# Performance work log

Measured on AMD Instinct MI355X. Metric: run time of the kernel, lower is better.

The kernel has to match this reference:

```python
import jax, jax.numpy as jnp
import numpy as np
import math

D_DIM = 512
N_HEAD = 8
HIDDEN = 2048
N_LAYERS = 4
CONTEXT = 64
MAX_LEN = 5000


def make_pe(d_model, max_len=MAX_LEN):
    position = np.arange(max_len)[:, None].astype(np.float32)
    div_term = np.exp(np.arange(0, d_model, 2).astype(np.float32) * (-math.log(10000.0) / d_model))
    pe = np.zeros((max_len, d_model), dtype=np.float32)
    pe[:, 0::2] = np.sin(position * div_term)
    pe[:, 1::2] = np.cos(position * div_term)
    return jnp.asarray(pe)


def setup_inputs() -> dict:
    key = jax.random.key(0)
    ks = jax.random.split(key, 64)
    B, T, IN = 16, 2048, 512
    inp = {}
    inp["trajectory"] = jax.random.normal(ks[0], (B, T, IN), dtype=jnp.float32)
    inp["obs_length"] = jax.random.randint(ks[1], (B,), 0, T)
    s = 0.02
    inp["w_in"] = jax.random.normal(ks[2], (IN, D_DIM), dtype=jnp.float32) * s
    inp["b_in"] = jnp.zeros((D_DIM,), dtype=jnp.float32)
    # per-layer params
    params = []
    ki = 3
    for l in range(N_LAYERS):
        p = {}
        p["w_qkv"] = jax.random.normal(ks[ki], (D_DIM, 3 * D_DIM), dtype=jnp.float32) * s; ki += 1
        p["b_qkv"] = jnp.zeros((3 * D_DIM,), dtype=jnp.float32)
        p["w_o"] = jax.random.normal(ks[ki], (D_DIM, D_DIM), dtype=jnp.float32) * s; ki += 1
        p["b_o"] = jnp.zeros((D_DIM,), dtype=jnp.float32)
        p["w_ff1"] = jax.random.normal(ks[ki], (D_DIM, HIDDEN), dtype=jnp.float32) * s; ki += 1
        p["b_ff1"] = jnp.zeros((HIDDEN,), dtype=jnp.float32)
        p["w_ff2"] = jax.random.normal(ks[ki], (HIDDEN, D_DIM), dtype=jnp.float32) * s; ki += 1
        p["b_ff2"] = jnp.zeros((D_DIM,), dtype=jnp.float32)
        p["ln1_g"] = jnp.ones((D_DIM,), dtype=jnp.float32)
        p["ln1_b"] = jnp.zeros((D_DIM,), dtype=jnp.float32)
        p["ln2_g"] = jnp.ones((D_DIM,), dtype=jnp.float32)
        p["ln2_b"] = jnp.zeros((D_DIM,), dtype=jnp.float32)
        for name, v in p.items():
            inp[f"L{l}_{name}"] = v
    return inp


def layer_norm(x, g, b, eps=1e-5):
    mu = jnp.mean(x, axis=-1, keepdims=True)
    var = jnp.mean((x - mu) ** 2, axis=-1, keepdims=True)
    return (x - mu) * jax.lax.rsqrt(var + eps) * g + b


def build_attn_mask(T, obs_length, context_length):
    # boolean mask, True = masked out. Causal + per-sample context window.
    i = jnp.arange(T)[:, None]
    j = jnp.arange(T)[None, :]
    causal = j > i  # (T, T)
    # window restriction applies for rows i with context_length < i < obs_length:
    # mask positions j <= i - context_length - 1, i.e. j < i - context_length
    window = j < (i - context_length)  # (T,T)
    row_active = (i[None, :, :] > context_length) & (i[None, :, :] < obs_length[:, None, None])  # (B,T,1)
    mask = causal[None] | (window[None] & row_active)  # (B,T,T)
    return mask


def encoder_layer(x, mask_add, pad_bool, p):
    B, T, D = x.shape
    H = N_HEAD
    Dh = D // H
    qkv = x @ p["w_qkv"] + p["b_qkv"]  # (B,T,3D)
    q, k, v = jnp.split(qkv, 3, axis=-1)
    q = q.reshape(B, T, H, Dh).transpose(0, 2, 1, 3)
    k = k.reshape(B, T, H, Dh).transpose(0, 2, 1, 3)
    v = v.reshape(B, T, H, Dh).transpose(0, 2, 1, 3)
    scores = jnp.einsum("bhqd,bhkd->bhqk", q, k) / jnp.sqrt(jnp.float32(Dh))
    scores = scores + mask_add[:, None] + pad_bool[:, None, None, :] * jnp.float32(-1e9)
    attn = jax.nn.softmax(scores, axis=-1)
    ctx = jnp.einsum("bhqk,bhkd->bhqd", attn, v)
    ctx = ctx.transpose(0, 2, 1, 3).reshape(B, T, D)
    attn_out = ctx @ p["w_o"] + p["b_o"]
    x = layer_norm(x + attn_out, p["ln1_g"], p["ln1_b"])
    ff = jax.nn.relu(x @ p["w_ff1"] + p["b_ff1"]) @ p["w_ff2"] + p["b_ff2"]
    x = layer_norm(x + ff, p["ln2_g"], p["ln2_b"])
    return x


def reference(trajectory, obs_length, w_in, b_in,
              L0_w_qkv, L0_b_qkv, L0_w_o, L0_b_o, L0_w_ff1, L0_b_ff1, L0_w_ff2, L0_b_ff2, L0_ln1_g, L0_ln1_b, L0_ln2_g, L0_ln2_b,
              L1_w_qkv, L1_b_qkv, L1_w_o, L1_b_o, L1_w_ff1, L1_b_ff1, L1_w_ff2, L1_b_ff2, L1_ln1_g, L1_ln1_b, L1_ln2_g, L1_ln2_b,
              L2_w_qkv, L2_b_qkv, L2_w_o, L2_b_o, L2_w_ff1, L2_b_ff1, L2_w_ff2, L2_b_ff2, L2_ln1_g, L2_ln1_b, L2_ln2_g, L2_ln2_b,
              L3_w_qkv, L3_b_qkv, L3_w_o, L3_b_o, L3_w_ff1, L3_b_ff1, L3_w_ff2, L3_b_ff2, L3_ln1_g, L3_ln1_b, L3_ln2_g, L3_ln2_b):
    B, T, _ = trajectory.shape
    pad = jnp.arange(T)[None, :] > obs_length[:, None]  # (B,T) True = pad
    x = trajectory @ w_in + b_in
    x = x + make_pe(D_DIM)[None, :T]
    mask_bool = build_attn_mask(T, obs_length, CONTEXT)  # (B,T,T)
    mask_add = jnp.where(mask_bool, jnp.float32(-1e9), jnp.float32(0.0))
    layers = [
        dict(w_qkv=L0_w_qkv, b_qkv=L0_b_qkv, w_o=L0_w_o, b_o=L0_b_o, w_ff1=L0_w_ff1, b_ff1=L0_b_ff1, w_ff2=L0_w_ff2, b_ff2=L0_b_ff2, ln1_g=L0_ln1_g, ln1_b=L0_ln1_b, ln2_g=L0_ln2_g, ln2_b=L0_ln2_b),
        dict(w_qkv=L1_w_qkv, b_qkv=L1_b_qkv, w_o=L1_w_o, b_o=L1_b_o, w_ff1=L1_w_ff1, b_ff1=L1_b_ff1, w_ff2=L1_w_ff2, b_ff2=L1_b_ff2, ln1_g=L1_ln1_g, ln1_b=L1_ln1_b, ln2_g=L1_ln2_g, ln2_b=L1_ln2_b),
        dict(w_qkv=L2_w_qkv, b_qkv=L2_b_qkv, w_o=L2_w_o, b_o=L2_b_o, w_ff1=L2_w_ff1, b_ff1=L2_b_ff1, w_ff2=L2_w_ff2, b_ff2=L2_b_ff2, ln1_g=L2_ln1_g, ln1_b=L2_ln1_b, ln2_g=L2_ln2_g, ln2_b=L2_ln2_b),
        dict(w_qkv=L3_w_qkv, b_qkv=L3_b_qkv, w_o=L3_w_o, b_o=L3_b_o, w_ff1=L3_w_ff1, b_ff1=L3_b_ff1, w_ff2=L3_w_ff2, b_ff2=L3_b_ff2, ln1_g=L3_ln1_g, ln1_b=L3_ln1_b, ln2_g=L3_ln2_g, ln2_b=L3_ln2_b),
    ]
    for p in layers:
        x = encoder_layer(x, mask_add, pad, p)
    # aggregate
    keep = ~pad
    x = x * keep[:, :, None]
    denom = jnp.sum(keep, axis=1).astype(x.dtype)[:, None]
    return jnp.sum(x, axis=1) / denom
```

## Files before the change

kernel.cpp:

```cpp
#include <hip/hip_runtime.h>

typedef unsigned short u16;
typedef unsigned int u32;
typedef __bf16 bf16x8 __attribute__((ext_vector_type(8)));
typedef float f32x4 __attribute__((ext_vector_type(4)));

#define MFMA16(a, b, c) __builtin_amdgcn_mfma_f32_16x16x32_bf16((a), (b), (c), 0, 0, 0)

__device__ __forceinline__ u16 f2bf(float x) {
    union { float f; u32 u; } v; v.f = x;
    u32 r = v.u + 0x7fffu + ((v.u >> 16) & 1u);
    return (u16)(r >> 16);
}
__device__ __forceinline__ float bf2f(u16 x) {
    union { u32 u; float f; } v; v.u = ((u32)x) << 16; return v.f;
}

typedef const __attribute__((address_space(1))) u32* gas1_t;
typedef __attribute__((address_space(3))) u32* las3_t;
__device__ __forceinline__ void g2lds16(const void* g, void* l) {
    __builtin_amdgcn_global_load_lds((gas1_t)g, (las3_t)l, 16, 0, 0);
}

template <int MODE, int BK>
__global__ __launch_bounds__(256) void gemm_bf16(
    const u16* __restrict__ A, const u16* __restrict__ BT,
    const float* __restrict__ bias, float* __restrict__ outF,
    u16* __restrict__ outB, const float* __restrict__ aux,
    const int* __restrict__ obs,
    int M, int N, int K)
{
    __shared__ u16 As[2][128 * BK];
    __shared__ u16 Bs[2][128 * BK];
    const int tid = threadIdx.x;
    const int w = tid >> 6, l = tid & 63;
    const int gx = gridDim.x, gy = gridDim.y;
    const int orig = blockIdx.y * gx + blockIdx.x;
    int tm, tn;
    if ((gy & 15) == 0) {
        const int xcd = orig & 7;
        const int loc = orig >> 3;
        tn = loc % gx;
        const int j = loc / gx;
        const int bb = j >> 1;
        tm = bb * 16 + ((xcd - bb) & 7) + ((j & 1) << 3);
    } else {
        tm = blockIdx.y; tn = blockIdx.x;
    }
    const int bm = tm * 128, bn = tn * 128;
    if ((bm & 2047) > obs[bm >> 11]) return;
    const int wr = (w >> 1) * 64, wc = (w & 1) * 64;
    f32x4 acc[4][4] = {};
    const int lane15 = l & 15, lhi = l >> 4;

    const int larow = l >> 2, lacol = (l & 3) * 8;
    const int r0a = 16 * w, r0b = 16 * (w + 4);
    const u16* Ap = &A[(size_t)(bm + larow) * K + lacol];
    const u16* Bp = &BT[(size_t)(bn + larow) * K + lacol];
    const int srow = l >> 3;
    const int scol = ((l & 7) ^ srow) << 3;

    auto STAGE = [&](int buf, int kt) {
        if constexpr (BK == 32) {
            g2lds16(Ap + (size_t)r0a * K + kt, &As[buf][r0a * 32]);
            g2lds16(Bp + (size_t)r0a * K + kt, &Bs[buf][r0a * 32]);
            g2lds16(Ap + (size_t)r0b * K + kt, &As[buf][r0b * 32]);
            g2lds16(Bp + (size_t)r0b * K + kt, &Bs[buf][r0b * 32]);
        } else {
            #pragma unroll
            for (int q = 0; q < 4; ++q) {
                const int rr = w * 32 + q * 8;
                g2lds16(&A[(size_t)(bm + rr + srow) * K + kt + scol], &As[buf][rr * 64]);
                g2lds16(&BT[(size_t)(bn + rr + srow) * K + kt + scol], &Bs[buf][rr * 64]);
            }
        }
    };

    STAGE(0, 0);
    __syncthreads();
    int cur = 0;
    const int nk = K / BK;
    for (int ki = 0; ki < nk; ++ki) {
        if (ki + 1 < nk) STAGE(cur ^ 1, (ki + 1) * BK);
        if constexpr (BK == 32) {
            bf16x8 af[4], bfr[4];
            #pragma unroll
            for (int i = 0; i < 4; ++i)
                af[i] = *(const bf16x8*)&As[cur][(wr + i * 16 + lane15) * 32 + 8 * lhi];
            #pragma unroll
            for (int j = 0; j < 4; ++j)
                bfr[j] = *(const bf16x8*)&Bs[cur][(wc + j * 16 + lane15) * 32 + 8 * lhi];
            #pragma unroll
            for (int i = 0; i < 4; ++i)
                #pragma unroll
                for (int j = 0; j < 4; ++j)
                    acc[i][j] = MFMA16(af[i], bfr[j], acc[i][j]);
        } else {
            #pragma unroll
            for (int kk = 0; kk < 2; ++kk) {
                const int gsw = ((kk * 4 + lhi) ^ (l & 7)) << 3;
                bf16x8 af[4], bfr[4];
                #pragma unroll
                for (int i = 0; i < 4; ++i)
                    af[i] = *(const bf16x8*)&As[cur][(wr + i * 16 + lane15) * 64 + gsw];
                #pragma unroll
                for (int j = 0; j < 4; ++j)
                    bfr[j] = *(const bf16x8*)&Bs[cur][(wc + j * 16 + lane15) * 64 + gsw];
                #pragma unroll
                for (int i = 0; i < 4; ++i)
                    #pragma unroll
                    for (int j = 0; j < 4; ++j)
                        acc[i][j] = MFMA16(af[i], bfr[j], acc[i][j]);
            }
        }
        __syncthreads();
        cur ^= 1;
    }

    const int r0 = bm + wr + lhi * 4;
    const int c0 = bn + wc + lane15;
    #pragma unroll
    for (int i = 0; i < 4; ++i) {
        #pragma unroll
        for (int j = 0; j < 4; ++j) {
            const int col = c0 + j * 16;
            const float bc = bias[col];
            #pragma unroll
            for (int r = 0; r < 4; ++r) {
                const int row = r0 + i * 16 + r;
                const size_t idx = (size_t)row * N + col;
                float val = acc[i][j][r] + bc;
                if constexpr (MODE == 0) {
                    val += aux[(size_t)(row & 2047) * 512 + col];
                    outF[idx] = val;
                    outB[idx] = f2bf(val);
                } else if constexpr (MODE == 1) {
                    outB[idx] = f2bf(val);
                } else if constexpr (MODE == 2) {
                    outF[idx] = val + aux[idx];
                } else {
                    outB[idx] = f2bf(fmaxf(val, 0.f));
                }
            }
        }
    }
}

__global__ void pe_kernel(float* __restrict__ PE) {
    const int idx = blockIdx.x * 256 + threadIdx.x;
    const int t = idx >> 8, p = idx & 255;
    const float fr = expf((float)(2 * p) * -0.017988946039015984f);
    const float arg = (float)t * fr;
    float s, c;
    sincosf(arg, &s, &c);
    float2 v = {s, c};
    *(float2*)&PE[(size_t)t * 512 + 2 * p] = v;
}

__global__ __launch_bounds__(256) void attn_kernel(
    const u16* __restrict__ QKV, u16* __restrict__ CTX, const int* __restrict__ obs,
    float* __restrict__ PBm, float* __restrict__ PBl, float* __restrict__ PBo)
{
    __shared__ u16 Ks[64 * 64];
    __shared__ u16 Vt[64 * 64];
    __shared__ u16 Ps[4][16 * 64];
    const int b = blockIdx.z, h = blockIdx.y;
    const int L = obs[b];
    const int tid = threadIdx.x, w = tid >> 6, l = tid & 63;
    const size_t tb = (size_t)b * 2048;

    if (blockIdx.x >= 32) {
        const int cbase = (blockIdx.x - 32) * 4;
        if (cbase * 64 > L) return;
        const int cc = cbase + w;
        float* pP = (float*)Ks;
        u16 q16[64];
        #pragma unroll
        for (int dd = 0; dd < 8; ++dd)
            *(uint4*)&q16[dd * 8] = *(const uint4*)&QKV[(tb + L) * 1536 + h * 64 + dd * 8];
        const int j = cc * 64 + l;
        const bool val = (j <= L);
        float s = -3.0e38f;
        if (val) {
            s = 0.f;
            const u16* kp = &QKV[(tb + j) * 1536 + 512 + h * 64];
            #pragma unroll
            for (int dd = 0; dd < 8; ++dd) {
                uint4 kk = *(const uint4*)&kp[dd * 8];
                const u16* ke = (const u16*)&kk;
                #pragma unroll
                for (int e = 0; e < 8; ++e)
                    s += bf2f(q16[dd * 8 + e]) * bf2f(ke[e]);
            }
            s *= 0.125f;
        }
        float mx = s;
        #pragma unroll
        for (int d = 1; d < 64; d <<= 1) mx = fmaxf(mx, __shfl_xor(mx, d, 64));
        const float p = val ? __expf(s - mx) : 0.f;
        float ps = p;
        #pragma unroll
        for (int d = 1; d < 64; d <<= 1) ps += __shfl_xor(ps, d, 64);
        pP[w * 64 + l] = p;
        __builtin_amdgcn_wave_barrier();
        if (cc * 64 <= L) {
            float oacc = 0.f;
            #pragma unroll 4
            for (int jj = 0; jj < 64; ++jj) {
                const int key = cc * 64 + jj;
                const int rr = (key <= L) ? key : L;
                oacc += pP[w * 64 + jj] * bf2f(QKV[(tb + rr) * 1536 + 1024 + h * 64 + l]);
            }
            const int pidx = (b * 8 + h) * 32 + cc;
            PBo[(size_t)pidx * 64 + l] = oacc;
            if (l == 0) { PBm[pidx] = mx; PBl[pidx] = ps; }
        }
        return;
    }

    const int i0 = blockIdx.x * 64;
    if (i0 > L) return;

    bf16x8 qa0, qa1;
    {
        const int qrow = i0 + 16 * w + (l & 15);
        const u16* qp = &QKV[(tb + qrow) * 1536 + h * 64];
        qa0 = *(const bf16x8*)(qp + 8 * (l >> 4));
        qa1 = *(const bf16x8*)(qp + 32 + 8 * (l >> 4));
    }
    const int g0 = (l >> 4) ^ (l & 7);
    const int g1 = ((l >> 4) + 4) ^ (l & 7);

    float m_r[4] = {-1e30f, -1e30f, -1e30f, -1e30f};
    float l_r[4] = {0.f, 0.f, 0.f, 0.f};
    f32x4 acc_o[4] = {};
    const int klo = (i0 >= 128) ? (i0 - 64) : 0;
    int khi = (L < klo) ? klo : min(i0 + 63, L);

    for (int j0 = klo; j0 <= khi; j0 += 64) {
        __syncthreads();
        {
            const int krow0 = 8 * w + (l >> 3);
            const int kswz = ((l & 7) ^ (l >> 3)) << 3;
            #pragma unroll
            for (int q = 0; q < 2; ++q) {
                const int row = krow0 + 32 * q;
                g2lds16(&QKV[(tb + j0 + row) * 1536 + 512 + h * 64 + kswz],
                        &Ks[(8 * w + 32 * q) * 64]);
            }
            const int vr = tid >> 3, c8 = (tid & 7) * 8;
            #pragma unroll
            for (int q = 0; q < 2; ++q) {
                const int row = vr + 32 * q;
                uint4 vv = *(const uint4*)&QKV[(tb + j0 + row) * 1536 + 1024 + h * 64 + c8];
                const u16* vs = (const u16*)&vv;
                #pragma unroll
                for (int e = 0; e < 8; ++e) {
                    const int d = c8 + e;
                    Vt[d * 64 + (((row >> 3) ^ e) << 3) + (row & 7)] = vs[e];
                }
            }
        }
        __syncthreads();
        f32x4 s[4];
        #pragma unroll
        for (int f = 0; f < 4; ++f) {
            f32x4 z = {0.f, 0.f, 0.f, 0.f};
            const int rowk = (f * 16 + (l & 15)) * 64;
            bf16x8 kb0 = *(const bf16x8*)&Ks[rowk + g0 * 8];
            bf16x8 kb1 = *(const bf16x8*)&Ks[rowk + g1 * 8];
            z = MFMA16(qa0, kb0, z);
            z = MFMA16(qa1, kb1, z);
            s[f] = z;
        }
        float pm[4];
        #pragma unroll
        for (int r = 0; r < 4; ++r) {
            const int i_r = i0 + 16 * w + (l >> 4) * 4 + r;
            float mx = -__builtin_inff();
            #pragma unroll
            for (int f = 0; f < 4; ++f) {
                const int j = j0 + f * 16 + (l & 15);
                float sv = s[f][r] * 0.125f;
                const bool ok = (i_r >= L) ? (j == klo)
                              : (j <= i_r && (i_r <= 64 || j >= i_r - 64));
                sv = ok ? sv : -__builtin_inff();
                s[f][r] = sv;
                mx = fmaxf(mx, sv);
            }
            pm[r] = mx;
        }
        #pragma unroll
        for (int d = 1; d < 16; d <<= 1)
            #pragma unroll
            for (int r = 0; r < 4; ++r) pm[r] = fmaxf(pm[r], __shfl_xor(pm[r], d, 64));
        float sc[4];
        #pragma unroll
        for (int r = 0; r < 4; ++r) {
            const float mn = fmaxf(m_r[r], fmaxf(pm[r], -1e30f));
            sc[r] = __expf(m_r[r] - mn);
            m_r[r] = mn;
            l_r[r] *= sc[r];
        }
        #pragma unroll
        for (int f = 0; f < 4; ++f)
            #pragma unroll
            for (int r = 0; r < 4; ++r) acc_o[f][r] *= sc[r];
        float ps[4] = {0.f, 0.f, 0.f, 0.f};
        #pragma unroll
        for (int f = 0; f < 4; ++f)
            #pragma unroll
            for (int r = 0; r < 4; ++r) {
                const float p = __expf(s[f][r] - m_r[r]);
                s[f][r] = p;
                ps[r] += p;
            }
        #pragma unroll
        for (int d = 1; d < 16; d <<= 1)
            #pragma unroll
            for (int r = 0; r < 4; ++r) ps[r] += __shfl_xor(ps[r], d, 64);
        #pragma unroll
        for (int r = 0; r < 4; ++r) l_r[r] += ps[r];
        {
            const int cg = ((l >> 3) & 1);
            #pragma unroll
            for (int f = 0; f < 4; ++f)
                #pragma unroll
                for (int r = 0; r < 4; ++r) {
                    const int prow = (l >> 4) * 4 + r;
                    Ps[w][prow * 64 + (((f * 2 + cg) ^ (prow & 7)) << 3) + (l & 7)] =
                        f2bf(s[f][r]);
                }
        }
        bf16x8 pa0 = *(const bf16x8*)&Ps[w][(l & 15) * 64 + g0 * 8];
        bf16x8 pa1 = *(const bf16x8*)&Ps[w][(l & 15) * 64 + g1 * 8];
        #pragma unroll
        for (int f = 0; f < 4; ++f) {
            const int dv = (f * 16 + (l & 15)) * 64;
            bf16x8 vb0 = *(const bf16x8*)&Vt[dv + g0 * 8];
            bf16x8 vb1 = *(const bf16x8*)&Vt[dv + g1 * 8];
            acc_o[f] = MFMA16(pa0, vb0, acc_o[f]);
            acc_o[f] = MFMA16(pa1, vb1, acc_o[f]);
        }
    }
    #pragma unroll
    for (int r = 0; r < 4; ++r) {
        const float inv = 1.f / l_r[r];
        const int row = i0 + 16 * w + (l >> 4) * 4 + r;
        if (row != L) {
            #pragma unroll
            for (int f = 0; f < 4; ++f)
                CTX[(tb + row) * 512 + h * 64 + f * 16 + (l & 15)] = f2bf(acc_o[f][r] * inv);
        }
    }
}

__global__ void attn_merge(const float* __restrict__ PBm, const float* __restrict__ PBl,
                           const float* __restrict__ PBo, u16* __restrict__ CTX,
                           const int* __restrict__ obs)
{
    const int h = blockIdx.x, b = blockIdx.y, l = threadIdx.x;
    const int L = obs[b];
    const int nc = (L >> 6) + 1;
    const int base = (b * 8 + h) * 32;
    float m = -3.0e38f;
    for (int c = 0; c < nc; ++c) m = fmaxf(m, PBm[base + c]);
    float lt = 0.f, ot = 0.f;
    for (int c = 0; c < nc; ++c) {
        const float sc = __expf(PBm[base + c] - m);
        lt += sc * PBl[base + c];
        ot += sc * PBo[(size_t)(base + c) * 64 + l];
    }
    CTX[((size_t)b * 2048 + L) * 512 + h * 64 + l] = f2bf(ot / lt);
}

__global__ __launch_bounds__(256) void ln_kernel(
    const float* __restrict__ Y, const float* __restrict__ gw,
    const float* __restrict__ bw, float* __restrict__ X, u16* __restrict__ Xb,
    const int* __restrict__ obs)
{
    const int tok0 = blockIdx.x * 4;
    if ((tok0 & 2047) > obs[tok0 >> 11]) return;
    const int tok = tok0 + (threadIdx.x >> 6);
    const int l = threadIdx.x & 63;
    const float* y = &Y[(size_t)tok * 512 + l * 8];
    f32x4 v0 = *(const f32x4*)y;
    f32x4 v1 = *(const f32x4*)(y + 4);
    float s = 0.f, sq = 0.f;
    #pragma unroll
    for (int e = 0; e < 4; ++e) {
        s += v0[e] + v1[e];
        sq += v0[e] * v0[e] + v1[e] * v1[e];
    }
    #pragma unroll
    for (int d = 1; d < 64; d <<= 1) {
        s += __shfl_xor(s, d, 64);
        sq += __shfl_xor(sq, d, 64);
    }
    const float mean = s * (1.f / 512.f);
    const float var = sq * (1.f / 512.f) - mean * mean;
    const float rstd = rsqrtf(var + 1e-5f);
    f32x4 o0, o1;
    union { u16 us[8]; uint4 u4; } pk;
    #pragma unroll
    for (int e = 0; e < 8; ++e) {
        const int d = l * 8 + e;
        const float xv = (e < 4) ? v0[e] : v1[e - 4];
        const float ov = (xv - mean) * rstd * gw[d] + bw[d];
        if (e < 4) o0[e] = ov; else o1[e - 4] = ov;
        pk.us[e] = f2bf(ov);
    }
    float* xo = &X[(size_t)tok * 512 + l * 8];
    *(f32x4*)xo = o0;
    *(f32x4*)(xo + 4) = o1;
    *(uint4*)&Xb[(size_t)tok * 512 + l * 8] = pk.u4;
}

__global__ void cast_bf16_kernel(const float* __restrict__ in, u16* __restrict__ out, int n) {
    const int i = (blockIdx.x * 256 + threadIdx.x) * 4;
    if (i + 3 < n) {
        f32x4 v = *(const f32x4*)&in[i];
        union { u16 us[4]; uint2 u2; } pk;
        #pragma unroll
        for (int e = 0; e < 4; ++e) pk.us[e] = f2bf(v[e]);
        *(uint2*)&out[i] = pk.u2;
    }
}

__global__ void transpose_cast(const float* __restrict__ W, u16* __restrict__ WT, int K, int N) {
    __shared__ float t[32][33];
    const int n0 = blockIdx.x * 32, k0 = blockIdx.y * 32;
    const int tx = threadIdx.x, ty = threadIdx.y;
    #pragma unroll
    for (int r = 0; r < 32; r += 8)
        t[ty + r][tx] = W[(size_t)(k0 + ty + r) * N + n0 + tx];
    __syncthreads();
    #pragma unroll
    for (int r = 0; r < 32; r += 8)
        WT[(size_t)(n0 + ty + r) * K + k0 + tx] = f2bf(t[tx][ty + r]);
}

struct WPack { const float* src[16]; u16* dst[16]; };
__global__ void transpose_all(WPack p) {
    __shared__ float t[32][33];
    int id = blockIdx.x;
    const int lyr = id / 3072;
    id -= lyr * 3072;
    int wi, K, N;
    if (id < 768)       { wi = 0; K = 512;  N = 1536; }
    else if (id < 1024) { wi = 1; K = 512;  N = 512;  id -= 768; }
    else if (id < 2048) { wi = 2; K = 512;  N = 2048; id -= 1024; }
    else                { wi = 3; K = 2048; N = 512;  id -= 2048; }
    const float* W = p.src[lyr * 4 + wi];
    u16* D = p.dst[lyr * 4 + wi];
    const int nx = N >> 5;
    const int n0 = (id % nx) * 32, k0 = (id / nx) * 32;
    const int tx = threadIdx.x, ty = threadIdx.y;
    #pragma unroll
    for (int r = 0; r < 32; r += 8)
        t[ty + r][tx] = W[(size_t)(k0 + ty + r) * N + n0 + tx];
    __syncthreads();
    #pragma unroll
    for (int r = 0; r < 32; r += 8)
        D[(size_t)(n0 + ty + r) * K + k0 + tx] = f2bf(t[tx][ty + r]);
}

__global__ void agg_partial(const float* __restrict__ X, float* __restrict__ part,
                            const int* __restrict__ obs) {
    const int b = blockIdx.y, c = blockIdx.x, d = threadIdx.x;
    const int L = obs[b];
    float s = 0.f;
    const int t0 = c * 128;
    int tend = t0 + 128;
    if (tend > L + 1) tend = L + 1;
    for (int t = t0; t < tend; ++t) s += X[((size_t)b * 2048 + t) * 512 + d];
    part[((size_t)b * 16 + c) * 512 + d] = s;
}

__global__ void agg_final(const float* __restrict__ part, float* __restrict__ out,
                          const int* __restrict__ obs) {
    const int b = blockIdx.x, d = threadIdx.x;
    float s = 0.f;
    #pragma unroll
    for (int c = 0; c < 16; ++c) s += part[((size_t)b * 16 + c) * 512 + d];
    out[b * 512 + d] = s / (float)(obs[b] + 1);
}

extern "C" void kernel_launch(void* const* d_in, const int* in_sizes, int n_in,
                              void* d_out, int out_size, void* d_ws, size_t ws_size,
                              hipStream_t stream)
{
    const int M = 32768;
    const int FCH = 16384;
    const bool bigws = ws_size >= (size_t)270 * 1024 * 1024;
    const float* traj = (const float*)d_in[0];
    const int* obs = (const int*)d_in[1];
    const float* w_in = (const float*)d_in[2];
    const float* b_in = (const float*)d_in[3];

    char* base = (char*)d_ws;
    size_t off = 0;
    auto carve = [&](size_t bytes) -> void* {
        void* p = base + off;
        off += (bytes + 255) & ~(size_t)255;
        return p;
    };
    u16* U     = (u16*)carve((size_t)M * (bigws ? 2048 : 1536) * 2);
    u16* Xb    = (u16*)carve((size_t)M * 512 * 2);
    float* X   = (float*)carve((size_t)M * 512 * 4);
    float* PE  = (float*)carve((size_t)2048 * 512 * 4);
    float* PBm = (float*)carve((size_t)16 * 8 * 32 * 4);
    float* PBl = (float*)carve((size_t)16 * 8 * 32 * 4);
    float* PBo = (float*)carve((size_t)16 * 8 * 32 * 64 * 4);
    float* part = (float*)carve((size_t)16 * 16 * 512 * 4);
    u16* wTin  = (u16*)carve((size_t)512 * 512 * 2);
    u16 *wqkv[4], *wo[4], *wff1[4], *wff2[4];
    for (int l = 0; l < 4; ++l) {
        wqkv[l] = (u16*)carve((size_t)1536 * 512 * 2);
        wo[l]   = (u16*)carve((size_t)512 * 512 * 2);
        wff1[l] = (u16*)carve((size_t)2048 * 512 * 2);
        wff2[l] = (u16*)carve((size_t)512 * 2048 * 2);
    }

    dim3 tb32(32, 8);
    pe_kernel<<<2048, 256, 0, stream>>>(PE);
    transpose_cast<<<dim3(16, 16), tb32, 0, stream>>>(w_in, wTin, 512, 512);
    {
        WPack p;
        for (int l = 0; l < 4; ++l) {
            const int bi = 4 + 12 * l;
            p.src[l * 4 + 0] = (const float*)d_in[bi + 0];
            p.src[l * 4 + 1] = (const float*)d_in[bi + 2];
            p.src[l * 4 + 2] = (const float*)d_in[bi + 4];
            p.src[l * 4 + 3] = (const float*)d_in[bi + 6];
            p.dst[l * 4 + 0] = wqkv[l];
            p.dst[l * 4 + 1] = wo[l];
            p.dst[l * 4 + 2] = wff1[l];
            p.dst[l * 4 + 3] = wff2[l];
        }
        transpose_all<<<12288, tb32, 0, stream>>>(p);
    }

    cast_bf16_kernel<<<(M * 512) / 1024, 256, 0, stream>>>(traj, U, M * 512);
    gemm_bf16<0, 64><<<dim3(4, M / 128), 256, 0, stream>>>(
        U, wTin, b_in, X, Xb, PE, obs, M, 512, 512);

    for (int lyr = 0; lyr < 4; ++lyr) {
        const int bi = 4 + 12 * lyr;
        const float* b_qkv = (const float*)d_in[bi + 1];
        const float* b_o   = (const float*)d_in[bi + 3];
        const float* b_ff1 = (const float*)d_in[bi + 5];
        const float* b_ff2 = (const float*)d_in[bi + 7];
        const float* ln1g  = (const float*)d_in[bi + 8];
        const float* ln1b  = (const float*)d_in[bi + 9];
        const float* ln2g  = (const float*)d_in[bi + 10];
        const float* ln2b  = (const float*)d_in[bi + 11];

        gemm_bf16<1, 32><<<dim3(12, M / 128), 256, 0, stream>>>(
            Xb, wqkv[lyr], b_qkv, nullptr, U, nullptr, obs, M, 1536, 512);
        attn_kernel<<<dim3(40, 8, 16), 256, 0, stream>>>(U, Xb, obs, PBm, PBl, PBo);
        attn_merge<<<dim3(8, 16), 64, 0, stream>>>(PBm, PBl, PBo, Xb, obs);
        gemm_bf16<2, 64><<<dim3(4, M / 128), 256, 0, stream>>>(
            Xb, wo[lyr], b_o, X, nullptr, X, obs, M, 512, 512);
        ln_kernel<<<M / 4, 256, 0, stream>>>(X, ln1g, ln1b, X, Xb, obs);
        if (bigws) {
            gemm_bf16<3, 32><<<dim3(16, M / 128), 256, 0, stream>>>(
                Xb, wff1[lyr], b_ff1, nullptr, U, nullptr, obs, M, 2048, 512);
            gemm_bf16<2, 64><<<dim3(4, M / 128), 256, 0, stream>>>(
                U, wff2[lyr], b_ff2, X, nullptr, X, obs, M, 512, 2048);
        } else {
            for (int c = 0; c < 2; ++c) {
                gemm_bf16<3, 32><<<dim3(16, FCH / 128), 256, 0, stream>>>(
                    Xb + (size_t)c * FCH * 512, wff1[lyr], b_ff1, nullptr, U, nullptr,
                    obs + c * 8, FCH, 2048, 512);
                gemm_bf16<2, 64><<<dim3(4, FCH / 128), 256, 0, stream>>>(
                    U, wff2[lyr], b_ff2, X + (size_t)c * FCH * 512, nullptr,
                    X + (size_t)c * FCH * 512, obs + c * 8, FCH, 512, 2048);
            }
        }
        ln_kernel<<<M / 4, 256, 0, stream>>>(X, ln2g, ln2b, X, Xb, obs);
    }

    agg_partial<<<dim3(16, 16), 512, 0, stream>>>(X, part, obs);
    agg_final<<<16, 512, 0, stream>>>(part, (float*)d_out, obs);
}
```

Measured before the change: 1.267 ms.

## Fuse output-projection and FFN2 GEMMs with residual add and LayerNorm

Adds a gemm_ln kernel in which each block computes a full 32x512 row strip, so it can add bias and residual and apply LayerNorm in the epilogue with a cross-wave reduction through shared memory. It replaces the W_o and FF2 GEMMs plus both standalone ln_kernel launches. This removes one full fp32 activation write and read and one launch per LayerNorm. In exchange the tiles are small in M (32 rows) and each block streams the whole 512-wide weight slice, which lowers weight reuse and may lower occupancy given the larger LDS footprint.

```diff
diff --git a/kernel.cpp b/kernel.cpp
--- a/kernel.cpp
+++ b/kernel.cpp
@@ -136,11 +136,129 @@
                     outB[idx] = f2bf(val);
                 } else if constexpr (MODE == 1) {
                     outB[idx] = f2bf(val);
-                } else if constexpr (MODE == 2) {
-                    outF[idx] = val + aux[idx];
                 } else {
                     outB[idx] = f2bf(fmaxf(val, 0.f));
                 }
+            }
+        }
+    }
+}
+
+__global__ __launch_bounds__(256) void gemm_ln(
+    const u16* __restrict__ A, const u16* __restrict__ BT,
+    const float* __restrict__ bias, const float* __restrict__ resid,
+    const float* __restrict__ gw, const float* __restrict__ bw,
+    float* __restrict__ X, u16* __restrict__ Xb,
+    const int* __restrict__ obs, int K)
+{
+    __shared__ u16 As[2][32 * 32];
+    __shared__ u16 Bs[2][512 * 32];
+    __shared__ float red[4][32][2];
+    const int tid = threadIdx.x;
+    const int w = tid >> 6, l = tid & 63;
+    const int bm = blockIdx.x * 32;
+    if ((bm & 2047) > obs[bm >> 11]) return;
+    const int lane15 = l & 15, lhi = l >> 4;
+    f32x4 acc[2][8] = {};
+
+    auto STAGE = [&](int buf, int kt) {
+        if (w < 2)
+            g2lds16(&A[(size_t)(bm + 16 * w + (l >> 2)) * K + kt + (l & 3) * 8],
+                    &As[buf][16 * w * 32]);
+        #pragma unroll
+        for (int q = 0; q < 8; ++q) {
+            const int n0 = (w * 8 + q) * 16;
+            g2lds16(&BT[(size_t)(n0 + (l >> 2)) * K + kt + (l & 3) * 8],
+                    &Bs[buf][n0 * 32]);
+        }
+    };
+
+    STAGE(0, 0);
+    __syncthreads();
+    int cur = 0;
+    const int nk = K >> 5;
+    for (int ki = 0; ki < nk; ++ki) {
+        if (ki + 1 < nk) STAGE(cur ^ 1, (ki + 1) << 5);
+        bf16x8 af[2], bfr[8];
+        #pragma unroll
+        for (int i = 0; i < 2; ++i)
+            af[i] = *(const bf16x8*)&As[cur][(i * 16 + lane15) * 32 + 8 * lhi];
+        #pragma unroll
+        for (int j = 0; j < 8; ++j)
+            bfr[j] = *(const bf16x8*)&Bs[cur][(w * 128 + j * 16 + lane15) * 32 + 8 * lhi];
+        #pragma unroll
+        for (int i = 0; i < 2; ++i)
+            #pragma unroll
+            for (int j = 0; j < 8; ++j)
+                acc[i][j] = MFMA16(af[i], bfr[j], acc[i][j]);
+        __syncthreads();
+        cur ^= 1;
+    }
+
+    const int c0 = w * 128 + lane15;
+    float sm[2][4] = {}, sq[2][4] = {};
+    #pragma unroll
+    for (int i = 0; i < 2; ++i) {
+        #pragma unroll
+        for (int j = 0; j < 8; ++j) {
+            const int col = c0 + j * 16;
+            const float bc = bias[col];
+            #pragma unroll
+            for (int r = 0; r < 4; ++r) {
+                const int row = bm + i * 16 + lhi * 4 + r;
+                float v = acc[i][j][r] + bc + resid[(size_t)row * 512 + col];
+                acc[i][j][r] = v;
+                sm[i][r] += v;
+                sq[i][r] += v * v;
+            }
+        }
+    }
+    #pragma unroll
+    for (int d = 1; d < 16; d <<= 1) {
+        #pragma unroll
+        for (int i = 0; i < 2; ++i)
+            #pragma unroll
+            for (int r = 0; r < 4; ++r) {
+                sm[i][r] += __shfl_xor(sm[i][r], d, 64);
+                sq[i][r] += __shfl_xor(sq[i][r], d, 64);
+            }
+    }
+    if (lane15 == 0) {
+        #pragma unroll
+        for (int i = 0; i < 2; ++i)
+            #pragma unroll
+            for (int r = 0; r < 4; ++r) {
+                const int rl = i * 16 + lhi * 4 + r;
+                red[w][rl][0] = sm[i][r];
+                red[w][rl][1] = sq[i][r];
+            }
+    }
+    __syncthreads();
+    float mean[2][4], rstd[2][4];
+    #pragma unroll
+    for (int i = 0; i < 2; ++i)
+        #pragma unroll
+        for (int r = 0; r < 4; ++r) {
+            const int rl = i * 16 + lhi * 4 + r;
+            const float s = red[0][rl][0] + red[1][rl][0] + red[2][rl][0] + red[3][rl][0];
+            const float q2 = red[0][rl][1] + red[1][rl][1] + red[2][rl][1] + red[3][rl][1];
+            const float mu = s * (1.f / 512.f);
+            const float var = q2 * (1.f / 512.f) - mu * mu;
+            mean[i][r] = mu;
+            rstd[i][r] = rsqrtf(var + 1e-5f);
+        }
+    #pragma unroll
+    for (int i = 0; i < 2; ++i) {
+        #pragma unroll
+        for (int j = 0; j < 8; ++j) {
+            const int col = c0 + j * 16;
+            const float g = gw[col], bb = bw[col];
+            #pragma unroll
+            for (int r = 0; r < 4; ++r) {
+                const int row = bm + i * 16 + lhi * 4 + r;
+                const float ov = (acc[i][j][r] - mean[i][r]) * rstd[i][r] * g + bb;
+                X[(size_t)row * 512 + col] = ov;
+                Xb[(size_t)row * 512 + col] = f2bf(ov);
             }
         }
     }
@@ -372,48 +490,6 @@
         ot += sc * PBo[(size_t)(base + c) * 64 + l];
     }
     CTX[((size_t)b * 2048 + L) * 512 + h * 64 + l] = f2bf(ot / lt);
-}
-
-__global__ __launch_bounds__(256) void ln_kernel(
-    const float* __restrict__ Y, const float* __restrict__ gw,
-    const float* __restrict__ bw, float* __restrict__ X, u16* __restrict__ Xb,
-    const int* __restrict__ obs)
-{
-    const int tok0 = blockIdx.x * 4;
-    if ((tok0 & 2047) > obs[tok0 >> 11]) return;
-    const int tok = tok0 + (threadIdx.x >> 6);
-    const int l = threadIdx.x & 63;
-    const float* y = &Y[(size_t)tok * 512 + l * 8];
-    f32x4 v0 = *(const f32x4*)y;
-    f32x4 v1 = *(const f32x4*)(y + 4);
-    float s = 0.f, sq = 0.f;
-    #pragma unroll
-    for (int e = 0; e < 4; ++e) {
-        s += v0[e] + v1[e];
-        sq += v0[e] * v0[e] + v1[e] * v1[e];
-    }
-    #pragma unroll
-    for (int d = 1; d < 64; d <<= 1) {
-        s += __shfl_xor(s, d, 64);
-        sq += __shfl_xor(sq, d, 64);
-    }
-    const float mean = s * (1.f / 512.f);
-    const float var = sq * (1.f / 512.f) - mean * mean;
-    const float rstd = rsqrtf(var + 1e-5f);
-    f32x4 o0, o1;
-    union { u16 us[8]; uint4 u4; } pk;
-    #pragma unroll
-    for (int e = 0; e < 8; ++e) {
-        const int d = l * 8 + e;
-        const float xv = (e < 4) ? v0[e] : v1[e - 4];
-        const float ov = (xv - mean) * rstd * gw[d] + bw[d];
-        if (e < 4) o0[e] = ov; else o1[e - 4] = ov;
-        pk.us[e] = f2bf(ov);
-    }
-    float* xo = &X[(size_t)tok * 512 + l * 8];
-    *(f32x4*)xo = o0;
-    *(f32x4*)(xo + 4) = o1;
-    *(uint4*)&Xb[(size_t)tok * 512 + l * 8] = pk.u4;
 }
 
 __global__ void cast_bf16_kernel(const float* __restrict__ in, u16* __restrict__ out, int n) {
@@ -560,25 +636,24 @@
             Xb, wqkv[lyr], b_qkv, nullptr, U, nullptr, obs, M, 1536, 512);
         attn_kernel<<<dim3(40, 8, 16), 256, 0, stream>>>(U, Xb, obs, PBm, PBl, PBo);
         attn_merge<<<dim3(8, 16), 64, 0, stream>>>(PBm, PBl, PBo, Xb, obs);
-        gemm_bf16<2, 64><<<dim3(4, M / 128), 256, 0, stream>>>(
-            Xb, wo[lyr], b_o, X, nullptr, X, obs, M, 512, 512);
-        ln_kernel<<<M / 4, 256, 0, stream>>>(X, ln1g, ln1b, X, Xb, obs);
+        gemm_ln<<<M / 32, 256, 0, stream>>>(
+            Xb, wo[lyr], b_o, X, ln1g, ln1b, X, Xb, obs, 512);
         if (bigws) {
             gemm_bf16<3, 32><<<dim3(16, M / 128), 256, 0, stream>>>(
                 Xb, wff1[lyr], b_ff1, nullptr, U, nullptr, obs, M, 2048, 512);
-            gemm_bf16<2, 64><<<dim3(4, M / 128), 256, 0, stream>>>(
-                U, wff2[lyr], b_ff2, X, nullptr, X, obs, M, 512, 2048);
+            gemm_ln<<<M / 32, 256, 0, stream>>>(
+                U, wff2[lyr], b_ff2, X, ln2g, ln2b, X, Xb, obs, 2048);
         } else {
             for (int c = 0; c < 2; ++c) {
                 gemm_bf16<3, 32><<<dim3(16, FCH / 128), 256, 0, stream>>>(
                     Xb + (size_t)c * FCH * 512, wff1[lyr], b_ff1, nullptr, U, nullptr,
                     obs + c * 8, FCH, 2048, 512);
-                gemm_bf16<2, 64><<<dim3(4, FCH / 128), 256, 0, stream>>>(
-                    U, wff2[lyr], b_ff2, X + (size_t)c * FCH * 512, nullptr,
-                    X + (size_t)c * FCH * 512, obs + c * 8, FCH, 512, 2048);
-            }
-        }
-        ln_kernel<<<M / 4, 256, 0, stream>>>(X, ln2g, ln2b, X, Xb, obs);
+                gemm_ln<<<FCH / 32, 256, 0, stream>>>(
+                    U, wff2[lyr], b_ff2, X + (size_t)c * FCH * 512, ln2g, ln2b,
+                    X + (size_t)c * FCH * 512, Xb + (size_t)c * FCH * 512,
+                    obs + c * 8, 2048);
+            }
+        }
     }
 
     agg_partial<<<dim3(16, 16), 512, 0, stream>>>(X, part, obs);
```

Result: slower. 1.457 ms (+15.0%).
